# Optimization experiments

Hardware: AMD Instinct MI355X
Metric: run time of the kernel (lower is better)

## Reference

```python
import jax, jax.numpy as jnp
import numpy as np

N = 50000
E = 800000
F_IN = 128
H = 8        # heads
C = 32       # hidden_channels per head
HC = H * C   # 256
NEG_SLOPE = 0.2


def setup_inputs() -> dict:
    key = jax.random.key(0)
    ks = jax.random.split(key, 16)
    s = 0.1
    return {
        'x': jax.random.normal(ks[0], (N, F_IN), jnp.float32),
        'edge_index': jax.random.randint(ks[1], (2, E), 0, N, jnp.int64),
        'edge_weights': jax.random.uniform(ks[2], (E,), jnp.float32),
        'W1': jax.random.normal(ks[3], (F_IN, HC), jnp.float32) * s,
        'att_src1': jax.random.normal(ks[4], (H, C), jnp.float32) * s,
        'att_dst1': jax.random.normal(ks[5], (H, C), jnp.float32) * s,
        'b1': jnp.zeros((HC,), jnp.float32),
        'W2': jax.random.normal(ks[6], (HC, HC), jnp.float32) * s,
        'att_src2': jax.random.normal(ks[7], (H, C), jnp.float32) * s,
        'att_dst2': jax.random.normal(ks[8], (H, C), jnp.float32) * s,
        'b2': jnp.zeros((HC,), jnp.float32),
        'We': jax.random.normal(ks[9], (HC, 1), jnp.float32) * s,
        'be': jnp.zeros((1,), jnp.float32),
        'Wn': jax.random.normal(ks[10], (HC, 1), jnp.float32) * s,
        'bn': jnp.zeros((1,), jnp.float32),
    }


def gat_conv(x, src, dst, W, att_src, att_dst, bias):
    """PyG GATConv (concat=True, eval mode, self-loops already in src/dst)."""
    n = x.shape[0]
    h = (x @ W).reshape(n, H, C)                      # [N,H,C]
    a_s = jnp.sum(h * att_src, axis=-1)               # [N,H]
    a_d = jnp.sum(h * att_dst, axis=-1)               # [N,H]
    e = jax.nn.leaky_relu(a_s[src] + a_d[dst], NEG_SLOPE)  # [E',H]
    m = jax.ops.segment_max(e, dst, num_segments=n)   # segment softmax over dst
    ex = jnp.exp(e - m[dst])
    denom = jax.ops.segment_sum(ex, dst, num_segments=n)
    alpha = ex / (denom[dst] + 1e-16)                 # [E',H]
    out = jax.ops.segment_sum(alpha[..., None] * h[src], dst, num_segments=n)
    return out.reshape(n, HC) + bias


def reference(x, edge_index, edge_weights, W1, att_src1, att_dst1, b1,
              W2, att_src2, att_dst2, b2, We, be, Wn, bn):
    src0, dst0 = edge_index[0], edge_index[1]
    loops = jnp.arange(N, dtype=src0.dtype)
    src = jnp.concatenate([src0, loops])
    dst = jnp.concatenate([dst0, loops])
    # edge_weights is passed to GATConv as edge_attr but unused (edge_dim=None)
    h = jax.nn.relu(gat_conv(x, src, dst, W1, att_src1, att_dst1, b1))
    h = jax.nn.relu(gat_conv(h, src, dst, W2, att_src2, att_dst2, b2))
    edge_pred = (h[src0] * h[dst0]) @ We + be          # [E,1]
    node_pred = h @ Wn + bn                            # [N,1]
    return (edge_pred, node_pred)
```

## Files before the change

kernel.cpp:

```cpp
#include <hip/hip_runtime.h>
#include <hip/hip_bf16.h>

#define NN 50000
#define NE 800000
#define FIN 128
#define HC 256
#define NEG_SLOPE 0.2f
#define LOG2E 1.4426950408889634f

#define GEMM_BLOCKS 1564
#define NSCAT 3328
#define NB_HIST 782
#define NB_W1 128
#define NB_W2 256
#define ELLS 64

typedef short bf16x8 __attribute__((ext_vector_type(8)));
typedef float f32x4 __attribute__((ext_vector_type(4)));

__device__ __forceinline__ unsigned short f2bf(float f) {
  unsigned u = __float_as_uint(f);
  u += 0x7fff + ((u >> 16) & 1);
  return (unsigned short)(u >> 16);
}
__device__ __forceinline__ float bf2f(unsigned short s) {
  return __uint_as_float((unsigned)s << 16);
}
__device__ __forceinline__ float bflo(unsigned u) { return __uint_as_float(u << 16); }
__device__ __forceinline__ float bfhi(unsigned u) { return __uint_as_float(u & 0xffff0000u); }

__global__ __launch_bounds__(256) void prep_hist(
    const float* __restrict__ W1, unsigned short* __restrict__ W1th,
    unsigned short* __restrict__ W1tl, const float* __restrict__ W2,
    unsigned short* __restrict__ W2th, unsigned short* __restrict__ W2tl,
    const int* __restrict__ ei, int* __restrict__ counts, int* __restrict__ rank,
    unsigned* __restrict__ gA, unsigned* __restrict__ gB, float* __restrict__ asg) {
  int b = blockIdx.x, t = threadIdx.x;
  if (b < NB_HIST) {
#pragma unroll
    for (int u = 0; u < 4; ++u) {
      int e = b * 1024 + u * 256 + t;
      if (e < NE) rank[e] = atomicAdd(&counts[ei[NE + e]], 1);
    }
  } else if (b < NB_HIST + NB_W1) {
    int j = (b - NB_HIST) * 256 + t;
    int n = j >> 7, k = j & 127;
    float v = W1[k * HC + n];
    unsigned short h = f2bf(v);
    W1th[j] = h;
    W1tl[j] = f2bf(v - bf2f(h));
  } else if (b < NB_HIST + NB_W1 + NB_W2) {
    int j = (b - NB_HIST - NB_W1) * 256 + t;
    int n = j >> 8, k = j & 255;
    float v = W2[k * HC + n];
    unsigned short h = f2bf(v);
    W2th[j] = h;
    W2tl[j] = f2bf(v - bf2f(h));
  } else {
    if (t < 128) { gA[t] = 0; gB[t] = 0; }
    if (t < 8) asg[t] = -1e30f;
  }
}

__global__ __launch_bounds__(256) void gemm_coef(
    const unsigned short* __restrict__ A, const float* __restrict__ Af,
    const unsigned short* __restrict__ Bth, const unsigned short* __restrict__ Btl,
    const float* __restrict__ att_s, const float* __restrict__ att_d,
    unsigned short* __restrict__ Cb, float* __restrict__ a_s,
    float* __restrict__ a_d, int M, int K,
    const int* __restrict__ ei, const int* __restrict__ cnts,
    const int* __restrict__ rank, int2* __restrict__ ce, int gemmN) {
  __shared__ unsigned short sA[64 * 40];
  __shared__ unsigned short sBh[128 * 40];
  __shared__ unsigned short sBl[128 * 40];
  __shared__ float sCS[64][4];
  __shared__ float sCD[64][4];

  int bid = blockIdx.x, t = threadIdx.x;
  if (bid >= gemmN) {
    int sid = bid - gemmN;
    int x = sid & 7;
    int c = sid >> 3;
#pragma unroll
    for (int u = 0; u < 8; ++u) {
      int e = c * 2048 + u * 256 + t;
      if (e < NE + NN) {
        int d = (e < NE) ? ei[NE + e] : e - NE;
        if ((unsigned)d / 6250u == (unsigned)x) {
          if (e < NE) {
            ce[d * ELLS + rank[e]] = make_int2(ei[e], e);
          } else {
            int cnt = cnts[d];
            int pad8 = (cnt + 8) & ~7;
            ce[d * ELLS + cnt] = make_int2(d, -1);
            for (int p = cnt + 1; p < pad8; ++p)
              ce[d * ELLS + p] = make_int2(-1, -1);
          }
        }
      }
    }
    return;
  }

  int w = t >> 6, lane = t & 63;
  int quad = lane >> 4, lrow = lane & 15;
  int m0 = (bid >> 1) * 64, n0 = (bid & 1) * 128;
  int rm = (w & 1) * 32, cn = (w >> 1) * 64;

  f32x4 acc[2][4] = {};

  for (int k0 = 0; k0 < K; k0 += 32) {
    {
      int row = t >> 2, q = t & 3;
      int gm = m0 + row;
      if (gm >= M) gm = M - 1;
      if (Af) {
        const float4* xp = (const float4*)(Af + (size_t)gm * K + k0 + q * 8);
        float4 f0 = xp[0], f1 = xp[1];
        uint4 h;
        h.x = (unsigned)f2bf(f0.x) | ((unsigned)f2bf(f0.y) << 16);
        h.y = (unsigned)f2bf(f0.z) | ((unsigned)f2bf(f0.w) << 16);
        h.z = (unsigned)f2bf(f1.x) | ((unsigned)f2bf(f1.y) << 16);
        h.w = (unsigned)f2bf(f1.z) | ((unsigned)f2bf(f1.w) << 16);
        *(uint4*)(sA + row * 40 + q * 8) = h;
      } else {
        *(uint4*)(sA + row * 40 + q * 8) = *(const uint4*)(A + (size_t)gm * K + k0 + q * 8);
      }
    }
#pragma unroll
    for (int i = 0; i < 2; ++i) {
      int idx = t + i * 256;
      int row = idx >> 2, q = idx & 3;
      size_t gbx = (size_t)(n0 + row) * K + k0 + q * 8;
      *(uint4*)(sBh + row * 40 + q * 8) = *(const uint4*)(Bth + gbx);
      *(uint4*)(sBl + row * 40 + q * 8) = *(const uint4*)(Btl + gbx);
    }
    __syncthreads();

    bf16x8 fa[2];
#pragma unroll
    for (int mi = 0; mi < 2; ++mi)
      fa[mi] = *(const bf16x8*)(sA + (rm + mi * 16 + lrow) * 40 + quad * 8);
#pragma unroll
    for (int ni = 0; ni < 4; ++ni) {
      bf16x8 fbh = *(const bf16x8*)(sBh + (cn + ni * 16 + lrow) * 40 + quad * 8);
      bf16x8 fbl = *(const bf16x8*)(sBl + (cn + ni * 16 + lrow) * 40 + quad * 8);
#pragma unroll
      for (int mi = 0; mi < 2; ++mi) {
        acc[mi][ni] = __builtin_amdgcn_mfma_f32_16x16x32_bf16(fa[mi], fbh, acc[mi][ni], 0, 0, 0);
        acc[mi][ni] = __builtin_amdgcn_mfma_f32_16x16x32_bf16(fa[mi], fbl, acc[mi][ni], 0, 0, 0);
      }
    }
    __syncthreads();
  }

  float vs[4], vd[4];
#pragma unroll
  for (int ni = 0; ni < 4; ++ni) {
    int gn = n0 + cn + ni * 16 + lrow;
    vs[ni] = att_s[gn] * LOG2E;
    vd[ni] = att_d[gn] * LOG2E;
  }
  int h4e = cn >> 5;

#pragma unroll
  for (int mi = 0; mi < 2; ++mi) {
#pragma unroll
    for (int r = 0; r < 4; ++r) {
      int lr = rm + mi * 16 + quad * 4 + r;
      int gm = m0 + lr;
      if (gm < M) {
#pragma unroll
        for (int ni = 0; ni < 4; ++ni) {
          int gn = n0 + cn + ni * 16 + lrow;
          Cb[(size_t)gm * HC + gn] = f2bf(acc[mi][ni][r]);
        }
      }
      float pse = acc[mi][0][r] * vs[0] + acc[mi][1][r] * vs[1];
      float pso = acc[mi][2][r] * vs[2] + acc[mi][3][r] * vs[3];
      float pde = acc[mi][0][r] * vd[0] + acc[mi][1][r] * vd[1];
      float pdo = acc[mi][2][r] * vd[2] + acc[mi][3][r] * vd[3];
#pragma unroll
      for (int off = 1; off <= 8; off <<= 1) {
        pse += __shfl_xor(pse, off);
        pso += __shfl_xor(pso, off);
        pde += __shfl_xor(pde, off);
        pdo += __shfl_xor(pdo, off);
      }
      if (lrow == 0) {
        sCS[lr][h4e] = pse;
        sCS[lr][h4e + 1] = pso;
        sCD[lr][h4e] = pde;
        sCD[lr][h4e + 1] = pdo;
      }
    }
  }
  __syncthreads();
  if (t < 64) {
    int gm = m0 + t;
    if (gm < M) {
      int o = (n0 >> 5);
      *(float4*)(a_s + (size_t)gm * 8 + o) = *(const float4*)&sCS[t][0];
      *(float4*)(a_d + (size_t)gm * 8 + o) = *(const float4*)&sCD[t][0];
    }
  }
}

__global__ __launch_bounds__(256) void agg_kernel(
    const unsigned short* __restrict__ htb, const float* __restrict__ a_s,
    const float* __restrict__ a_d, const int* __restrict__ cnts,
    const int2* __restrict__ ce, const float* __restrict__ bias,
    unsigned short* __restrict__ outb,
    const float* __restrict__ Wn, const float* __restrict__ bn,
    float* __restrict__ outn) {
  int d = blockIdx.x * 4 + (threadIdx.x >> 6);
  if (d >= NN) return;
  int l = threadIdx.x & 63;
  int hh = l >> 3;
  const uint2* ht2 = (const uint2*)htb;
  float adh = a_d[d * 8 + hh];
  int r0 = d * ELLS;
  int r1 = r0 + ((cnts[d] + 8) & ~7);
  float denom = 0.f;
  float4 acc = {0.f, 0.f, 0.f, 0.f};
  for (int r = r0; r < r1; r += 8) {
    const int4* cp = (const int4*)(ce + r);
    int4 c01 = cp[0], c23 = cp[1], c45 = cp[2], c67 = cp[3];
    int s[8] = {c01.x, c01.z, c23.x, c23.z, c45.x, c45.z, c67.x, c67.z};
    float as_[8];
    uint2 q[8];
#pragma unroll
    for (int j = 0; j < 8; ++j) {
      as_[j] = a_s[s[j] * 8 + hh];
      q[j] = ht2[s[j] * 64 + l];
    }
#pragma unroll
    for (int j = 0; j < 8; ++j) {
      float e = as_[j] + adh;
      e = fmaxf(e, NEG_SLOPE * e);
      float w = exp2f(e);
      denom += w;
      acc.x += w * bflo(q[j].x);
      acc.y += w * bfhi(q[j].x);
      acc.z += w * bflo(q[j].y);
      acc.w += w * bfhi(q[j].y);
    }
  }
  float dv = 1.f / denom;
  float4 bi = *(const float4*)(bias + l * 4);
  float4 o;
  o.x = fmaxf(fmaf(acc.x, dv, bi.x), 0.f);
  o.y = fmaxf(fmaf(acc.y, dv, bi.y), 0.f);
  o.z = fmaxf(fmaf(acc.z, dv, bi.z), 0.f);
  o.w = fmaxf(fmaf(acc.w, dv, bi.w), 0.f);
  uint2 pb;
  pb.x = (unsigned)f2bf(o.x) | ((unsigned)f2bf(o.y) << 16);
  pb.y = (unsigned)f2bf(o.z) | ((unsigned)f2bf(o.w) << 16);
  ((uint2*)outb)[d * 64 + l] = pb;
  if (outn) {
    float4 wv = *(const float4*)(Wn + l * 4);
    float p = o.x * wv.x + o.y * wv.y + o.z * wv.z + o.w * wv.w;
#pragma unroll
    for (int off = 1; off <= 32; off <<= 1) p += __shfl_xor(p, off);
    if (l == 0) outn[d] = p + bn[0];
  }
}

__global__ __launch_bounds__(256) void edge_pred_kernel(
    const unsigned short* __restrict__ h2b, const int* __restrict__ cnts,
    const int2* __restrict__ ce, const float* __restrict__ We,
    const float* __restrict__ be, float* __restrict__ out) {
  int d = blockIdx.x * 4 + (threadIdx.x >> 6);
  if (d >= NN) return;
  int lane = threadIdx.x & 63;
  int g = lane >> 4, l = lane & 15;
  float b = be[0];
  const uint4* h24 = (const uint4*)h2b;

  uint4 qd0 = h24[d * 32 + l * 2], qd1 = h24[d * 32 + l * 2 + 1];
  float wd[16];
  {
    const float4* wep = (const float4*)(We + l * 16);
    float4 w0 = wep[0], w1 = wep[1], w2 = wep[2], w3 = wep[3];
    wd[0] = bflo(qd0.x) * w0.x;  wd[1] = bfhi(qd0.x) * w0.y;
    wd[2] = bflo(qd0.y) * w0.z;  wd[3] = bfhi(qd0.y) * w0.w;
    wd[4] = bflo(qd0.z) * w1.x;  wd[5] = bfhi(qd0.z) * w1.y;
    wd[6] = bflo(qd0.w) * w1.z;  wd[7] = bfhi(qd0.w) * w1.w;
    wd[8] = bflo(qd1.x) * w2.x;  wd[9] = bfhi(qd1.x) * w2.y;
    wd[10] = bflo(qd1.y) * w2.z; wd[11] = bfhi(qd1.y) * w2.w;
    wd[12] = bflo(qd1.z) * w3.x; wd[13] = bfhi(qd1.z) * w3.y;
    wd[14] = bflo(qd1.w) * w3.z; wd[15] = bfhi(qd1.w) * w3.w;
  }

  int r0 = d * ELLS, r1 = r0 + cnts[d];
  for (int r = r0; r < r1; r += 16) {
    int rr[4];
    int ss[4], id[4];
#pragma unroll
    for (int j = 0; j < 4; ++j) {
      rr[j] = r + 4 * j + g;
      ss[j] = 0; id[j] = -1;
      if (rr[j] < r1) { int2 p = ce[rr[j]]; ss[j] = p.x; id[j] = p.y; }
    }
    uint4 a0[4], a1[4];
#pragma unroll
    for (int j = 0; j < 4; ++j) {
      a0[j] = h24[ss[j] * 32 + l * 2];
      a1[j] = h24[ss[j] * 32 + l * 2 + 1];
    }
    float p[4];
#pragma unroll
    for (int j = 0; j < 4; ++j) {
      p[j] = bflo(a0[j].x) * wd[0] + bfhi(a0[j].x) * wd[1] + bflo(a0[j].y) * wd[2] +
             bfhi(a0[j].y) * wd[3] + bflo(a0[j].z) * wd[4] + bfhi(a0[j].z) * wd[5] +
             bflo(a0[j].w) * wd[6] + bfhi(a0[j].w) * wd[7] + bflo(a1[j].x) * wd[8] +
             bfhi(a1[j].x) * wd[9] + bflo(a1[j].y) * wd[10] + bfhi(a1[j].y) * wd[11] +
             bflo(a1[j].z) * wd[12] + bfhi(a1[j].z) * wd[13] + bflo(a1[j].w) * wd[14] +
             bfhi(a1[j].w) * wd[15];
#pragma unroll
      for (int off = 1; off <= 8; off <<= 1) p[j] += __shfl_xor(p[j], off);
    }
    if (l == 0) {
#pragma unroll
      for (int j = 0; j < 4; ++j)
        if (id[j] >= 0) out[id[j]] = p[j] + b;
    }
  }
}

extern "C" void kernel_launch(void* const* d_in, const int* in_sizes, int n_in,
                              void* d_out, int out_size, void* d_ws, size_t ws_size,
                              hipStream_t stream) {
  const float* x  = (const float*)d_in[0];
  const int* ei   = (const int*)d_in[1];
  const float* W1 = (const float*)d_in[3];
  const float* as1 = (const float*)d_in[4];
  const float* ad1 = (const float*)d_in[5];
  const float* b1 = (const float*)d_in[6];
  const float* W2 = (const float*)d_in[7];
  const float* as2 = (const float*)d_in[8];
  const float* ad2 = (const float*)d_in[9];
  const float* b2 = (const float*)d_in[10];
  const float* We = (const float*)d_in[11];
  const float* be = (const float*)d_in[12];
  const float* Wn = (const float*)d_in[13];
  const float* bn = (const float*)d_in[14];
  float* out = (float*)d_out;

  char* wsp = (char*)d_ws;
  auto alloc = [&](size_t bytes) {
    char* p = wsp;
    wsp += (bytes + 255) & ~(size_t)255;
    return p;
  };
  unsigned short* hbAr = (unsigned short*)alloc((size_t)(NN + 1) * HC * 2);
  unsigned short* hbA = hbAr + HC;
  unsigned short* h1b = (unsigned short*)alloc((size_t)NN * HC * 2);
  unsigned short* hbBr = (unsigned short*)alloc((size_t)(NN + 1) * HC * 2);
  unsigned short* hbB = hbBr + HC;
  float* a_sr = (float*)alloc((size_t)(8 + NN * 8) * 4);
  float* a_s = a_sr + 8;
  float* a_d = (float*)alloc((size_t)NN * 8 * 4);
  int2* ce = (int2*)alloc((size_t)NN * ELLS * 8);
  int* counts = (int*)alloc((size_t)NN * 4);
  int* rank = (int*)alloc((size_t)NE * 4);
  unsigned short* W1th = (unsigned short*)alloc((size_t)FIN * HC * 2);
  unsigned short* W1tl = (unsigned short*)alloc((size_t)FIN * HC * 2);
  unsigned short* W2th = (unsigned short*)alloc((size_t)HC * HC * 2);
  unsigned short* W2tl = (unsigned short*)alloc((size_t)HC * HC * 2);

  hipMemsetAsync(counts, 0, (size_t)NN * 4, stream);

  prep_hist<<<NB_HIST + NB_W1 + NB_W2 + 1, 256, 0, stream>>>(
      W1, W1th, W1tl, W2, W2th, W2tl, ei, counts, rank,
      (unsigned*)hbAr, (unsigned*)hbBr, a_sr);

  gemm_coef<<<GEMM_BLOCKS + NSCAT, 256, 0, stream>>>(
      (const unsigned short*)nullptr, x, W1th, W1tl, as1, ad1, hbA, a_s, a_d,
      NN, FIN, ei, counts, rank, ce, GEMM_BLOCKS);
  agg_kernel<<<NN / 4, 256, 0, stream>>>(hbA, a_s, a_d, counts, ce, b1, h1b,
                                         (const float*)nullptr, (const float*)nullptr,
                                         (float*)nullptr);

  gemm_coef<<<GEMM_BLOCKS, 256, 0, stream>>>(
      h1b, (const float*)nullptr, W2th, W2tl, as2, ad2, hbA, a_s, a_d,
      NN, HC, (const int*)nullptr, counts, rank, ce, GEMM_BLOCKS);
  agg_kernel<<<NN / 4, 256, 0, stream>>>(hbA, a_s, a_d, counts, ce, b2, hbB,
                                         Wn, bn, out + NE);

  edge_pred_kernel<<<NN / 4, 256, 0, stream>>>(hbB, counts, ce, We, be, out);
}
```

Measured before the change: 411.2 us.

## Fuse layer-1 aggregation with layer-2 GEMM and attention coefficients

Adds an agg_gemm kernel that aggregates 64 destination nodes per 1024-thread block into shared memory and then runs the layer-2 bf16 hi/lo MFMA GEMM plus attention-coefficient reduction directly from that tile. This removes the round trip of the intermediate h1 buffer through global memory and one kernel launch. It also changes ELL padding and the aggregation unroll from 8 to 4, cutting wasted padded edge slots at the cost of less memory-level parallelism per iteration. The fused kernel runs only 782 large blocks, so occupancy and load balance across CUs may suffer.

```diff
diff --git a/kernel.cpp b/kernel.cpp
--- a/kernel.cpp
+++ b/kernel.cpp
@@ -9,6 +9,7 @@
 #define LOG2E 1.4426950408889634f
 
 #define GEMM_BLOCKS 1564
+#define FUSED_BLOCKS 782
 #define NSCAT 3328
 #define NB_HIST 782
 #define NB_W1 128
@@ -34,7 +35,8 @@
     unsigned short* __restrict__ W1tl, const float* __restrict__ W2,
     unsigned short* __restrict__ W2th, unsigned short* __restrict__ W2tl,
     const int* __restrict__ ei, int* __restrict__ counts, int* __restrict__ rank,
-    unsigned* __restrict__ gA, unsigned* __restrict__ gB, float* __restrict__ asg) {
+    unsigned* __restrict__ gA, unsigned* __restrict__ gC,
+    float* __restrict__ asg, float* __restrict__ asg2) {
   int b = blockIdx.x, t = threadIdx.x;
   if (b < NB_HIST) {
 #pragma unroll
@@ -57,13 +59,13 @@
     W2th[j] = h;
     W2tl[j] = f2bf(v - bf2f(h));
   } else {
-    if (t < 128) { gA[t] = 0; gB[t] = 0; }
-    if (t < 8) asg[t] = -1e30f;
+    if (t < 128) { gA[t] = 0; gC[t] = 0; }
+    if (t < 8) { asg[t] = -1e30f; asg2[t] = -1e30f; }
   }
 }
 
 __global__ __launch_bounds__(256) void gemm_coef(
-    const unsigned short* __restrict__ A, const float* __restrict__ Af,
+    const float* __restrict__ Af,
     const unsigned short* __restrict__ Bth, const unsigned short* __restrict__ Btl,
     const float* __restrict__ att_s, const float* __restrict__ att_d,
     unsigned short* __restrict__ Cb, float* __restrict__ a_s,
@@ -91,9 +93,9 @@
             ce[d * ELLS + rank[e]] = make_int2(ei[e], e);
           } else {
             int cnt = cnts[d];
-            int pad8 = (cnt + 8) & ~7;
+            int pad4 = (cnt + 4) & ~3;
             ce[d * ELLS + cnt] = make_int2(d, -1);
-            for (int p = cnt + 1; p < pad8; ++p)
+            for (int p = cnt + 1; p < pad4; ++p)
               ce[d * ELLS + p] = make_int2(-1, -1);
           }
         }
@@ -114,18 +116,14 @@
       int row = t >> 2, q = t & 3;
       int gm = m0 + row;
       if (gm >= M) gm = M - 1;
-      if (Af) {
-        const float4* xp = (const float4*)(Af + (size_t)gm * K + k0 + q * 8);
-        float4 f0 = xp[0], f1 = xp[1];
-        uint4 h;
-        h.x = (unsigned)f2bf(f0.x) | ((unsigned)f2bf(f0.y) << 16);
-        h.y = (unsigned)f2bf(f0.z) | ((unsigned)f2bf(f0.w) << 16);
-        h.z = (unsigned)f2bf(f1.x) | ((unsigned)f2bf(f1.y) << 16);
-        h.w = (unsigned)f2bf(f1.z) | ((unsigned)f2bf(f1.w) << 16);
-        *(uint4*)(sA + row * 40 + q * 8) = h;
-      } else {
-        *(uint4*)(sA + row * 40 + q * 8) = *(const uint4*)(A + (size_t)gm * K + k0 + q * 8);
-      }
+      const float4* xp = (const float4*)(Af + (size_t)gm * K + k0 + q * 8);
+      float4 f0 = xp[0], f1 = xp[1];
+      uint4 h;
+      h.x = (unsigned)f2bf(f0.x) | ((unsigned)f2bf(f0.y) << 16);
+      h.y = (unsigned)f2bf(f0.z) | ((unsigned)f2bf(f0.w) << 16);
+      h.z = (unsigned)f2bf(f1.x) | ((unsigned)f2bf(f1.y) << 16);
+      h.w = (unsigned)f2bf(f1.z) | ((unsigned)f2bf(f1.w) << 16);
+      *(uint4*)(sA + row * 40 + q * 8) = h;
     }
 #pragma unroll
     for (int i = 0; i < 2; ++i) {
@@ -202,6 +200,151 @@
       int o = (n0 >> 5);
       *(float4*)(a_s + (size_t)gm * 8 + o) = *(const float4*)&sCS[t][0];
       *(float4*)(a_d + (size_t)gm * 8 + o) = *(const float4*)&sCD[t][0];
+    }
+  }
+}
+
+__global__ __launch_bounds__(1024) void agg_gemm(
+    const unsigned short* __restrict__ htb, const float* __restrict__ a_s,
+    const float* __restrict__ a_d, const int* __restrict__ cnts,
+    const int2* __restrict__ ce, const float* __restrict__ bias,
+    const unsigned short* __restrict__ Bth, const unsigned short* __restrict__ Btl,
+    const float* __restrict__ att_s, const float* __restrict__ att_d,
+    unsigned short* __restrict__ Cb, float* __restrict__ a_s2,
+    float* __restrict__ a_d2) {
+  __shared__ unsigned short sH[64 * 264];
+  __shared__ unsigned short sBh[256 * 40];
+  __shared__ unsigned short sBl[256 * 40];
+  __shared__ float sCS[64][8];
+  __shared__ float sCD[64][8];
+
+  int t = threadIdx.x;
+  int w = t >> 6, lane = t & 63;
+  int m0 = blockIdx.x * 64;
+
+  {
+    int l = lane;
+    int hh = l >> 3;
+    const uint2* ht2 = (const uint2*)htb;
+    float4 bi = *(const float4*)(bias + l * 4);
+    for (int i = 0; i < 4; ++i) {
+      int lr = 4 * w + i;
+      int d = m0 + lr;
+      if (d < NN) {
+        float adh = a_d[d * 8 + hh];
+        int r0 = d * ELLS;
+        int r1 = r0 + ((cnts[d] + 4) & ~3);
+        float denom = 0.f;
+        float4 acc = {0.f, 0.f, 0.f, 0.f};
+        for (int r = r0; r < r1; r += 4) {
+          const int4* cp = (const int4*)(ce + r);
+          int4 c01 = cp[0], c23 = cp[1];
+          int s[4] = {c01.x, c01.z, c23.x, c23.z};
+          float as_[4];
+          uint2 q[4];
+#pragma unroll
+          for (int j = 0; j < 4; ++j) {
+            as_[j] = a_s[s[j] * 8 + hh];
+            q[j] = ht2[s[j] * 64 + l];
+          }
+#pragma unroll
+          for (int j = 0; j < 4; ++j) {
+            float e = as_[j] + adh;
+            e = fmaxf(e, NEG_SLOPE * e);
+            float wgt = exp2f(e);
+            denom += wgt;
+            acc.x += wgt * bflo(q[j].x);
+            acc.y += wgt * bfhi(q[j].x);
+            acc.z += wgt * bflo(q[j].y);
+            acc.w += wgt * bfhi(q[j].y);
+          }
+        }
+        float dv = 1.f / denom;
+        float4 o;
+        o.x = fmaxf(fmaf(acc.x, dv, bi.x), 0.f);
+        o.y = fmaxf(fmaf(acc.y, dv, bi.y), 0.f);
+        o.z = fmaxf(fmaf(acc.z, dv, bi.z), 0.f);
+        o.w = fmaxf(fmaf(acc.w, dv, bi.w), 0.f);
+        uint2 pb;
+        pb.x = (unsigned)f2bf(o.x) | ((unsigned)f2bf(o.y) << 16);
+        pb.y = (unsigned)f2bf(o.z) | ((unsigned)f2bf(o.w) << 16);
+        *(uint2*)(sH + lr * 264 + l * 4) = pb;
+      }
+    }
+  }
+  __syncthreads();
+
+  int wr = w >> 2, wc = w & 3;
+  int quad = lane >> 4, lrow = lane & 15;
+
+  f32x4 acc[4] = {};
+
+  for (int k0 = 0; k0 < HC; k0 += 32) {
+    {
+      int row = t >> 2, q = t & 3;
+      size_t gbx = (size_t)row * HC + k0 + q * 8;
+      *(uint4*)(sBh + row * 40 + q * 8) = *(const uint4*)(Bth + gbx);
+      *(uint4*)(sBl + row * 40 + q * 8) = *(const uint4*)(Btl + gbx);
+    }
+    __syncthreads();
+
+    bf16x8 fa = *(const bf16x8*)(sH + (wr * 16 + lrow) * 264 + k0 + quad * 8);
+#pragma unroll
+    for (int ni = 0; ni < 4; ++ni) {
+      int brow = wc * 64 + ni * 16 + lrow;
+      bf16x8 fbh = *(const bf16x8*)(sBh + brow * 40 + quad * 8);
+      bf16x8 fbl = *(const bf16x8*)(sBl + brow * 40 + quad * 8);
+      acc[ni] = __builtin_amdgcn_mfma_f32_16x16x32_bf16(fa, fbh, acc[ni], 0, 0, 0);
+      acc[ni] = __builtin_amdgcn_mfma_f32_16x16x32_bf16(fa, fbl, acc[ni], 0, 0, 0);
+    }
+    __syncthreads();
+  }
+
+  float vs[4], vd[4];
+#pragma unroll
+  for (int ni = 0; ni < 4; ++ni) {
+    int gn = wc * 64 + ni * 16 + lrow;
+    vs[ni] = att_s[gn] * LOG2E;
+    vd[ni] = att_d[gn] * LOG2E;
+  }
+  int h4e = wc * 2;
+
+#pragma unroll
+  for (int r = 0; r < 4; ++r) {
+    int lr = wr * 16 + quad * 4 + r;
+    int gm = m0 + lr;
+    if (gm < NN) {
+#pragma unroll
+      for (int ni = 0; ni < 4; ++ni) {
+        int gn = wc * 64 + ni * 16 + lrow;
+        Cb[(size_t)gm * HC + gn] = f2bf(acc[ni][r]);
+      }
+    }
+    float pse = acc[0][r] * vs[0] + acc[1][r] * vs[1];
+    float pso = acc[2][r] * vs[2] + acc[3][r] * vs[3];
+    float pde = acc[0][r] * vd[0] + acc[1][r] * vd[1];
+    float pdo = acc[2][r] * vd[2] + acc[3][r] * vd[3];
+#pragma unroll
+    for (int off = 1; off <= 8; off <<= 1) {
+      pse += __shfl_xor(pse, off);
+      pso += __shfl_xor(pso, off);
+      pde += __shfl_xor(pde, off);
+      pdo += __shfl_xor(pdo, off);
+    }
+    if (lrow == 0) {
+      sCS[lr][h4e] = pse;
+      sCS[lr][h4e + 1] = pso;
+      sCD[lr][h4e] = pde;
+      sCD[lr][h4e + 1] = pdo;
+    }
+  }
+  __syncthreads();
+  if (t < 128) {
+    int row = t >> 1, half = t & 1;
+    int gm = m0 + row;
+    if (gm < NN) {
+      *(float4*)(a_s2 + (size_t)gm * 8 + half * 4) = *(const float4*)&sCS[row][half * 4];
+      *(float4*)(a_d2 + (size_t)gm * 8 + half * 4) = *(const float4*)&sCD[row][half * 4];
     }
   }
 }
@@ -220,22 +363,22 @@
   const uint2* ht2 = (const uint2*)htb;
   float adh = a_d[d * 8 + hh];
   int r0 = d * ELLS;
-  int r1 = r0 + ((cnts[d] + 8) & ~7);
+  int r1 = r0 + ((cnts[d] + 4) & ~3);
   float denom = 0.f;
   float4 acc = {0.f, 0.f, 0.f, 0.f};
-  for (int r = r0; r < r1; r += 8) {
+  for (int r = r0; r < r1; r += 4) {
     const int4* cp = (const int4*)(ce + r);
-    int4 c01 = cp[0], c23 = cp[1], c45 = cp[2], c67 = cp[3];
-    int s[8] = {c01.x, c01.z, c23.x, c23.z, c45.x, c45.z, c67.x, c67.z};
-    float as_[8];
-    uint2 q[8];
-#pragma unroll
-    for (int j = 0; j < 8; ++j) {
+    int4 c01 = cp[0], c23 = cp[1];
+    int s[4] = {c01.x, c01.z, c23.x, c23.z};
+    float as_[4];
+    uint2 q[4];
+#pragma unroll
+    for (int j = 0; j < 4; ++j) {
       as_[j] = a_s[s[j] * 8 + hh];
       q[j] = ht2[s[j] * 64 + l];
     }
 #pragma unroll
-    for (int j = 0; j < 8; ++j) {
+    for (int j = 0; j < 4; ++j) {
       float e = as_[j] + adh;
       e = fmaxf(e, NEG_SLOPE * e);
       float w = exp2f(e);
@@ -294,13 +437,12 @@
 
   int r0 = d * ELLS, r1 = r0 + cnts[d];
   for (int r = r0; r < r1; r += 16) {
-    int rr[4];
     int ss[4], id[4];
 #pragma unroll
     for (int j = 0; j < 4; ++j) {
-      rr[j] = r + 4 * j + g;
+      int rr = r + 4 * j + g;
       ss[j] = 0; id[j] = -1;
-      if (rr[j] < r1) { int2 p = ce[rr[j]]; ss[j] = p.x; id[j] = p.y; }
+      if (rr < r1) { int2 p = ce[rr]; ss[j] = p.x; id[j] = p.y; }
     }
     uint4 a0[4], a1[4];
 #pragma unroll
@@ -355,12 +497,15 @@
   };
   unsigned short* hbAr = (unsigned short*)alloc((size_t)(NN + 1) * HC * 2);
   unsigned short* hbA = hbAr + HC;
-  unsigned short* h1b = (unsigned short*)alloc((size_t)NN * HC * 2);
-  unsigned short* hbBr = (unsigned short*)alloc((size_t)(NN + 1) * HC * 2);
-  unsigned short* hbB = hbBr + HC;
+  unsigned short* hbCr = (unsigned short*)alloc((size_t)(NN + 1) * HC * 2);
+  unsigned short* hbC = hbCr + HC;
+  unsigned short* hbB = hbA;
   float* a_sr = (float*)alloc((size_t)(8 + NN * 8) * 4);
   float* a_s = a_sr + 8;
   float* a_d = (float*)alloc((size_t)NN * 8 * 4);
+  float* a_s2r = (float*)alloc((size_t)(8 + NN * 8) * 4);
+  float* a_s2 = a_s2r + 8;
+  float* a_d2 = (float*)alloc((size_t)NN * 8 * 4);
   int2* ce = (int2*)alloc((size_t)NN * ELLS * 8);
   int* counts = (int*)alloc((size_t)NN * 4);
   int* rank = (int*)alloc((size_t)NE * 4);
@@ -373,19 +518,16 @@
 
   prep_hist<<<NB_HIST + NB_W1 + NB_W2 + 1, 256, 0, stream>>>(
       W1, W1th, W1tl, W2, W2th, W2tl, ei, counts, rank,
-      (unsigned*)hbAr, (unsigned*)hbBr, a_sr);
+      (unsigned*)hbAr, (unsigned*)hbCr, a_sr, a_s2r);
 
   gemm_coef<<<GEMM_BLOCKS + NSCAT, 256, 0, stream>>>(
-      (const unsigned short*)nullptr, x, W1th, W1tl, as1, ad1, hbA, a_s, a_d,
+      x, W1th, W1tl, as1, ad1, hbA, a_s, a_d,
       NN, FIN, ei, counts, rank, ce, GEMM_BLOCKS);
-  agg_kernel<<<NN / 4, 256, 0, stream>>>(hbA, a_s, a_d, counts, ce, b1, h1b,
-                                         (const float*)nullptr, (const float*)nullptr,
-                                         (float*)nullptr);
-
-  gemm_coef<<<GEMM_BLOCKS, 256, 0, stream>>>(
-      h1b, (const float*)nullptr, W2th, W2tl, as2, ad2, hbA, a_s, a_d,
-      NN, HC, (const int*)nullptr, counts, rank, ce, GEMM_BLOCKS);
-  agg_kernel<<<NN / 4, 256, 0, stream>>>(hbA, a_s, a_d, counts, ce, b2, hbB,
+
+  agg_gemm<<<FUSED_BLOCKS, 1024, 0, stream>>>(
+      hbA, a_s, a_d, counts, ce, b1, W2th, W2tl, as2, ad2, hbC, a_s2, a_d2);
+
+  agg_kernel<<<NN / 4, 256, 0, stream>>>(hbC, a_s2, a_d2, counts, ce, b2, hbB,
                                          Wn, bn, out + NE);
 
   edge_pred_kernel<<<NN / 4, 256, 0, stream>>>(hbB, counts, ce, We, be, out);
```

Measured after the change: 421.9 us. +2.6%, slower.
